# Kernel optimization log

Measured on AMD Instinct MI355X. Metric: run time of the kernel, lower is better.

The kernel has to match this reference:

```python
import math
import jax, jax.numpy as jnp
import numpy as np

H = 16          # head_count
DM = 1024       # model_dim
D = DM // H     # dim_per_head = 64
B, SL, CL = 2, 1024, 512


def setup_inputs() -> dict:
    key = jax.random.key(0)
    ks = jax.random.split(key, 16)
    s = 0.02  # weight init scale
    def W(k):
        return jax.random.normal(k, (DM, DM), jnp.float32) * s
    def b(k):
        return jax.random.normal(k, (DM,), jnp.float32) * s
    return {
        "self_kvq": jax.random.normal(ks[0], (B, SL, DM), jnp.float32),
        "ctx_kv": jax.random.normal(ks[1], (B, CL, DM), jnp.float32),
        "self_mask": jax.random.bernoulli(ks[2], 0.1, (B, SL, SL)),
        "ctx_mask": jax.random.bernoulli(ks[3], 0.1, (B, 1, CL)),
        "Wq": W(ks[4]), "bq": b(ks[5]),
        "Wks": W(ks[6]), "bks": b(ks[7]),
        "Wvs": W(ks[8]), "bvs": b(ks[9]),
        "Wkc": W(ks[10]), "bkc": b(ks[11]),
        "Wvc": W(ks[12]), "bvc": b(ks[13]),
        "ctx_bias": jnp.full((1,), -10.0, jnp.float32),  # Parameter(ones(1) * -10)
        "Wo": W(ks[14]), "bo": b(ks[15]),
    }


def reference(self_kvq, ctx_kv, self_mask, ctx_mask,
              Wq, bq, Wks, bks, Wvs, bvs, Wkc, bkc, Wvc, bvc,
              ctx_bias, Wo, bo):
    Bx, self_len, _ = self_kvq.shape
    ctx_len = ctx_kv.shape[1]

    def shape4(x):  # (B, L, DM) -> (B, H, L, D)
        return x.reshape(Bx, -1, H, D).transpose(0, 2, 1, 3)

    query = shape4(self_kvq @ Wq.T + bq) / math.sqrt(D)
    key = shape4(jnp.concatenate([self_kvq @ Wks.T + bks, ctx_kv @ Wkc.T + bkc], axis=1))
    value = shape4(jnp.concatenate([self_kvq @ Wvs.T + bvs, ctx_kv @ Wvc.T + bvc], axis=1))

    scores = jnp.einsum('bhqd,bhkd->bhqk', query, key)
    # ctx_weight_param: add learned bias to the context segment of the scores
    kidx = jnp.arange(self_len + ctx_len)
    scores = scores + jnp.where(kidx >= self_len, ctx_bias[0], jnp.zeros((), scores.dtype))
    scores = scores.astype(jnp.float32)

    # self_mask: (B, Q, self_len) -> (B, 1, Q, self_len); ctx_mask: (B, 1, ctx_len) -> (B, 1, Q, ctx_len)
    full_mask = jnp.concatenate([
        jnp.broadcast_to(self_mask[:, None], (Bx, 1, self_len, self_len)),
        jnp.broadcast_to(ctx_mask[:, None], (Bx, 1, self_len, ctx_len)),
    ], axis=-1)
    scores = jnp.where(full_mask, jnp.float32(-1e18), scores)

    attn = jax.nn.softmax(scores, axis=-1).astype(query.dtype)
    # dropout p=0.0 -> identity
    context = jnp.einsum('bhqk,bhkd->bhqd', attn, value)
    context = context.transpose(0, 2, 1, 3).reshape(Bx, self_len, H * D)
    output = context @ Wo.T + bo

    ctx_attn_probs = attn[..., self_len:]
    ctx_attn_probs = ctx_attn_probs / ctx_attn_probs.sum(axis=-1, keepdims=True)
    top_attn = ctx_attn_probs[:, 0]  # head 0: (B, Q, ctx_len)
    return output, top_attn, attn
```

## Files before the change

kernel.cpp:

```cpp
#include <hip/hip_runtime.h>
#include <cstdint>

constexpr int H  = 16;
constexpr int D  = 64;
constexpr int DM = 1024;
constexpr int B  = 2;
constexpr int SL = 1024;
constexpr int CL = 512;
constexpr int KL = SL + CL;
constexpr int SPAD = KL + 4;
constexpr size_t M1 = 1u << 20;

typedef short bf16x8  __attribute__((ext_vector_type(8)));
typedef float f32x4   __attribute__((ext_vector_type(4)));
typedef short short4v __attribute__((ext_vector_type(4)));

__device__ __forceinline__ short f2b(float f) {
    uint32_t u = __float_as_uint(f);
    u = (u + 0x7fffu + ((u >> 16) & 1u)) >> 16;
    return (short)u;
}

__device__ __forceinline__ bf16x8 ld8(const unsigned short* p) {
    return *reinterpret_cast<const bf16x8*>(p);
}

__device__ __forceinline__ void async16(const void* g, void* l) {
    __builtin_amdgcn_global_load_lds(
        (const __attribute__((address_space(1))) void*)g,
        (__attribute__((address_space(3))) void*)l,
        16, 0, 0);
}

struct ConvSrc { const float* p[8]; };

__global__ __launch_bounds__(256)
void convert_kernel(ConvSrc srcs, unsigned short* __restrict__ dst)
{
    size_t i8 = (size_t)blockIdx.x * 256 + threadIdx.x;
    size_t e  = i8 * 8;
    int u = (int)(e >> 20);
    const float* s; size_t off;
    if (u < 2) { s = srcs.p[0]; off = e; }
    else       { s = srcs.p[u - 1]; off = e - ((size_t)u << 20); }
    float4 a = *reinterpret_cast<const float4*>(s + off);
    float4 b = *reinterpret_cast<const float4*>(s + off + 4);
    bf16x8 r;
    r[0]=f2b(a.x); r[1]=f2b(a.y); r[2]=f2b(a.z); r[3]=f2b(a.w);
    r[4]=f2b(b.x); r[5]=f2b(b.y); r[6]=f2b(b.z); r[7]=f2b(b.w);
    *reinterpret_cast<bf16x8*>(dst + e) = r;
}

template<int MODE, int RPB_SHIFT, int OUTLEN, int ROWOFF>
__device__ __forceinline__ void gemm128_body(
    const unsigned short* __restrict__ A,
    const unsigned short* __restrict__ W,
    const float* __restrict__ bias,
    void* __restrict__ outp, float scale,
    unsigned short* sA, unsigned short* sB)
{
    const int t   = threadIdx.x;
    const int l   = t & 63;
    const int wid = t >> 6;
    const int wr  = wid >> 1, wc = wid & 1;
    const int lr  = l & 15,  lg = l >> 4;
    const int mbase = blockIdx.y * 128;
    const int nbase = blockIdx.x * 128;

    f32x4 acc[4][4] = {};
    for (int k0 = 0; k0 < DM; k0 += 32) {
        #pragma unroll
        for (int i = 0; i < 2; ++i) {
            int c   = t + 256 * i;
            int row = c >> 2, kc = (c & 3) * 8;
            async16(A + (size_t)(mbase + row) * DM + k0 + kc, sA + c * 8);
            async16(W + (size_t)(nbase + row) * DM + k0 + kc, sB + c * 8);
        }
        __syncthreads();
        bf16x8 af[4], bfr[4];
        #pragma unroll
        for (int i = 0; i < 4; ++i) {
            af[i]  = ld8(sA + (wr * 64 + i * 16 + lr) * 32 + lg * 8);
            bfr[i] = ld8(sB + (wc * 64 + i * 16 + lr) * 32 + lg * 8);
        }
        #pragma unroll
        for (int i = 0; i < 4; ++i)
            #pragma unroll
            for (int j = 0; j < 4; ++j)
                acc[i][j] = __builtin_amdgcn_mfma_f32_16x16x32_bf16(af[i], bfr[j], acc[i][j], 0, 0, 0);
        __syncthreads();
    }

    #pragma unroll
    for (int mi = 0; mi < 4; ++mi) {
        #pragma unroll
        for (int nj = 0; nj < 4; ++nj) {
            int n = nbase + wc * 64 + nj * 16 + lr;
            float bi = bias[n];
            if (MODE == 1) {
                int m0 = mbase + wr * 64 + mi * 16 + lg * 4;
                int bb = m0 >> RPB_SHIFT;
                int s0 = m0 & ((1 << RPB_SHIFT) - 1);
                int hh = n >> 6, dd = n & 63;
                unsigned short* o = (unsigned short*)outp +
                    ((size_t)(bb * H + hh) * D + dd) * KL + ROWOFF + s0;
                short4v pk;
                #pragma unroll
                for (int r = 0; r < 4; ++r) pk[r] = f2b((acc[mi][nj][r] + bi) * scale);
                *reinterpret_cast<short4v*>(o) = pk;
            } else {
                #pragma unroll
                for (int r = 0; r < 4; ++r) {
                    int m = mbase + wr * 64 + mi * 16 + lg * 4 + r;
                    float v = (acc[mi][nj][r] + bi) * scale;
                    if (MODE == 0) {
                        int bb = m >> RPB_SHIFT;
                        int s  = m & ((1 << RPB_SHIFT) - 1);
                        int hh = n >> 6, dd = n & 63;
                        ((unsigned short*)outp)[((size_t)(bb * H + hh) * OUTLEN + ROWOFF + s) * D + dd]
                            = (unsigned short)f2b(v);
                    } else {
                        ((float*)outp)[(size_t)m * DM + n] = v;
                    }
                }
            }
        }
    }
}

__global__ __launch_bounds__(256)
void self_proj_kernel(const unsigned short* __restrict__ Abf,
                      const unsigned short* __restrict__ Wq,
                      const unsigned short* __restrict__ Wks,
                      const unsigned short* __restrict__ Wvs,
                      const float* __restrict__ bq,
                      const float* __restrict__ bks,
                      const float* __restrict__ bvs,
                      unsigned short* __restrict__ q_ws,
                      unsigned short* __restrict__ k_ws,
                      unsigned short* __restrict__ vT_ws)
{
    __shared__ unsigned short sA[128 * 32];
    __shared__ unsigned short sB[128 * 32];
    if (blockIdx.z == 0)
        gemm128_body<0, 10, SL, 0>(Abf, Wq,  bq,  q_ws,  0.125f, sA, sB);
    else if (blockIdx.z == 1)
        gemm128_body<0, 10, KL, 0>(Abf, Wks, bks, k_ws,  1.0f,   sA, sB);
    else
        gemm128_body<1, 10, 0,  0>(Abf, Wvs, bvs, vT_ws, 1.0f,   sA, sB);
}

__global__ __launch_bounds__(256)
void ctx_proj_kernel(const unsigned short* __restrict__ Abf,
                     const unsigned short* __restrict__ Wkc,
                     const unsigned short* __restrict__ Wvc,
                     const float* __restrict__ bkc,
                     const float* __restrict__ bvc,
                     unsigned short* __restrict__ k_ws,
                     unsigned short* __restrict__ vT_ws)
{
    __shared__ unsigned short sA[128 * 32];
    __shared__ unsigned short sB[128 * 32];
    if (blockIdx.z == 0)
        gemm128_body<0, 9, KL, SL>(Abf, Wkc, bkc, k_ws,  1.0f, sA, sB);
    else
        gemm128_body<1, 9, 0,  SL>(Abf, Wvc, bvc, vT_ws, 1.0f, sA, sB);
}

__global__ __launch_bounds__(256)
void out_proj_kernel(const unsigned short* __restrict__ ctx_bf,
                     const unsigned short* __restrict__ Wo,
                     const float* __restrict__ bo,
                     float* __restrict__ out0)
{
    __shared__ unsigned short sA[128 * 32];
    __shared__ unsigned short sB[128 * 32];
    gemm128_body<2, 10, 0, 0>(ctx_bf, Wo, bo, out0, 1.0f, sA, sB);
}

__global__ __launch_bounds__(512)
void attn_kernel(const unsigned short* __restrict__ q_ws,
                 const unsigned short* __restrict__ k_ws,
                 const unsigned short* __restrict__ vT_ws,
                 const int* __restrict__ self_mask,
                 const int* __restrict__ ctx_mask,
                 const float* __restrict__ ctx_bias,
                 float* __restrict__ attn_out,
                 float* __restrict__ top_out,
                 unsigned short* __restrict__ ctx_ws)
{
    __shared__ float s_scores[16 * SPAD];
    __shared__ float s_rden[16];

    const int bid = blockIdx.x;
    const int bh  = bid & 31;
    const int qt  = bid >> 5;
    const int b   = bh >> 4;
    const int h   = bh & 15;
    const int t   = threadIdx.x;
    const int l   = t & 63;
    const int wid = t >> 6;
    const int lr  = l & 15;
    const int lg  = l >> 4;

    const unsigned short* qb = q_ws + (size_t)bh * SL * D + (size_t)qt * 16 * D;
    const unsigned short* kb = k_ws + (size_t)bh * KL * D;
    const unsigned short* vb = vT_ws + (size_t)bh * D * KL;

    bf16x8 aq0 = ld8(qb + lr * D + lg * 8);
    bf16x8 aq1 = ld8(qb + lr * D + 32 + lg * 8);

    for (int jj = 0; jj < 12; ++jj) {
        int j  = wid * 12 + jj;
        int kp = j * 16 + lr;
        bf16x8 bk0 = ld8(kb + (size_t)kp * D + lg * 8);
        bf16x8 bk1 = ld8(kb + (size_t)kp * D + 32 + lg * 8);
        f32x4 c = {};
        c = __builtin_amdgcn_mfma_f32_16x16x32_bf16(aq0, bk0, c, 0, 0, 0);
        c = __builtin_amdgcn_mfma_f32_16x16x32_bf16(aq1, bk1, c, 0, 0, 0);
        #pragma unroll
        for (int r = 0; r < 4; ++r)
            s_scores[(lg * 4 + r) * SPAD + j * 16 + lr] = c[r];
    }
    __syncthreads();

    {
        const int rr = t >> 5;
        const int c0 = t & 31;
        const int qg = qt * 16 + rr;
        const float cb = ctx_bias[0];
        const int4* smrow4 = (const int4*)(self_mask + ((size_t)b * SL + qg) * SL);
        const int4* cmrow4 = (const int4*)(ctx_mask + (size_t)b * CL);
        float* srow = s_scores + rr * SPAD;

        float4 ev[12];
        float mx = -3.0e38f;
        #pragma unroll
        for (int jj = 0; jj < 12; ++jj) {
            int c4 = c0 + jj * 32;
            float4 s = *reinterpret_cast<const float4*>(srow + c4 * 4);
            if (c4 < 256) {
                int4 m = smrow4[c4];
                if (m.x) s.x = -1e30f;
                if (m.y) s.y = -1e30f;
                if (m.z) s.z = -1e30f;
                if (m.w) s.w = -1e30f;
            } else {
                int4 m = cmrow4[c4 - 256];
                s.x += cb; s.y += cb; s.z += cb; s.w += cb;
                if (m.x) s.x = -1e30f;
                if (m.y) s.y = -1e30f;
                if (m.z) s.z = -1e30f;
                if (m.w) s.w = -1e30f;
            }
            ev[jj] = s;
            mx = fmaxf(mx, fmaxf(fmaxf(s.x, s.y), fmaxf(s.z, s.w)));
        }
        #pragma unroll
        for (int o = 1; o < 32; o <<= 1) mx = fmaxf(mx, __shfl_xor(mx, o));

        float sum = 0.f, csum = 0.f;
        #pragma unroll
        for (int jj = 0; jj < 12; ++jj) {
            int c4 = c0 + jj * 32;
            float4 s = ev[jj];
            float4 e;
            e.x = __expf(s.x - mx); e.y = __expf(s.y - mx);
            e.z = __expf(s.z - mx); e.w = __expf(s.w - mx);
            ev[jj] = e;
            *reinterpret_cast<float4*>(srow + c4 * 4) = e;
            float se = e.x + e.y + e.z + e.w;
            sum += se;
            if (c4 >= 256) csum += se;
        }
        #pragma unroll
        for (int o = 1; o < 32; o <<= 1) { sum += __shfl_xor(sum, o); csum += __shfl_xor(csum, o); }
        float rden = 1.0f / sum;
        float rcs  = 1.0f / csum;
        if (c0 == 0) s_rden[rr] = rden;

        float4* arow4 = (float4*)(attn_out + ((size_t)bh * SL + qg) * KL);
        float4* trow4 = (float4*)(top_out + ((size_t)b * SL + qg) * CL);
        #pragma unroll
        for (int jj = 0; jj < 12; ++jj) {
            int c4 = c0 + jj * 32;
            float4 e = ev[jj];
            float4 w; w.x = e.x * rden; w.y = e.y * rden; w.z = e.z * rden; w.w = e.w * rden;
            arow4[c4] = w;
            if (h == 0 && c4 >= 256) {
                float4 tw; tw.x = e.x * rcs; tw.y = e.y * rcs; tw.z = e.z * rcs; tw.w = e.w * rcs;
                trow4[c4 - 256] = tw;
            }
        }
    }
    __syncthreads();

    f32x4 accv[4] = {};
    for (int ks = 0; ks < 6; ++ks) {
        int k0 = wid * 192 + ks * 32;
        const float* prow = s_scores + lr * SPAD + k0 + lg * 8;
        float4 p0 = *reinterpret_cast<const float4*>(prow);
        float4 p1 = *reinterpret_cast<const float4*>(prow + 4);
        bf16x8 ap;
        ap[0]=f2b(p0.x); ap[1]=f2b(p0.y); ap[2]=f2b(p0.z); ap[3]=f2b(p0.w);
        ap[4]=f2b(p1.x); ap[5]=f2b(p1.y); ap[6]=f2b(p1.z); ap[7]=f2b(p1.w);
        #pragma unroll
        for (int df = 0; df < 4; ++df) {
            bf16x8 bv = ld8(vb + (size_t)(df * 16 + lr) * KL + k0 + lg * 8);
            accv[df] = __builtin_amdgcn_mfma_f32_16x16x32_bf16(ap, bv, accv[df], 0, 0, 0);
        }
    }
    __syncthreads();
    float* s_part = s_scores;
    #pragma unroll
    for (int df = 0; df < 4; ++df)
        #pragma unroll
        for (int r = 0; r < 4; ++r)
            s_part[wid * 1024 + (lg * 4 + r) * 64 + df * 16 + lr] = accv[df][r];
    __syncthreads();

    for (int i = t; i < 1024; i += 512) {
        int s = i >> 6, dd = i & 63;
        float v = 0.f;
        #pragma unroll
        for (int w = 0; w < 8; ++w) v += s_part[w * 1024 + i];
        v *= s_rden[s];
        ctx_ws[((size_t)b * SL + (size_t)qt * 16 + s) * DM + h * D + dd] = (unsigned short)f2b(v);
    }
}

extern "C" void kernel_launch(void* const* d_in, const int* in_sizes, int n_in,
                              void* d_out, int out_size, void* d_ws, size_t ws_size,
                              hipStream_t stream)
{
    const float* self_kvq = (const float*)d_in[0];
    const float* ctx_kv   = (const float*)d_in[1];
    const int*   self_mask= (const int*)d_in[2];
    const int*   ctx_mask = (const int*)d_in[3];
    const float* Wq  = (const float*)d_in[4];
    const float* bq  = (const float*)d_in[5];
    const float* Wks = (const float*)d_in[6];
    const float* bks = (const float*)d_in[7];
    const float* Wvs = (const float*)d_in[8];
    const float* bvs = (const float*)d_in[9];
    const float* Wkc = (const float*)d_in[10];
    const float* bkc = (const float*)d_in[11];
    const float* Wvc = (const float*)d_in[12];
    const float* bvc = (const float*)d_in[13];
    const float* ctx_bias = (const float*)d_in[14];
    const float* Wo  = (const float*)d_in[15];
    const float* bo  = (const float*)d_in[16];

    float* out0     = (float*)d_out;
    float* out_top  = out0 + (size_t)B * SL * DM;
    float* out_attn = out_top + (size_t)B * SL * CL;

    unsigned short* wsp  = (unsigned short*)d_ws;
    unsigned short* Abf_self = wsp + 0 * M1;
    unsigned short* Abf_ctx  = wsp + 2 * M1;
    unsigned short* Wq_b     = wsp + 3 * M1;
    unsigned short* Wks_b    = wsp + 4 * M1;
    unsigned short* Wvs_b    = wsp + 5 * M1;
    unsigned short* Wkc_b    = wsp + 6 * M1;
    unsigned short* Wvc_b    = wsp + 7 * M1;
    unsigned short* Wo_b     = wsp + 8 * M1;
    unsigned short* q_ws     = wsp + 9 * M1;
    unsigned short* k_ws     = wsp + 11 * M1;
    unsigned short* vT_ws    = wsp + 14 * M1;
    unsigned short* ctx_ws   = wsp + 0;

    ConvSrc cs;
    cs.p[0] = self_kvq; cs.p[1] = ctx_kv;
    cs.p[2] = Wq; cs.p[3] = Wks; cs.p[4] = Wvs;
    cs.p[5] = Wkc; cs.p[6] = Wvc; cs.p[7] = Wo;
    convert_kernel<<<4608, 256, 0, stream>>>(cs, wsp);

    self_proj_kernel<<<dim3(8, 16, 3), 256, 0, stream>>>(
        Abf_self, Wq_b, Wks_b, Wvs_b, bq, bks, bvs, q_ws, k_ws, vT_ws);
    ctx_proj_kernel<<<dim3(8, 8, 2), 256, 0, stream>>>(
        Abf_ctx, Wkc_b, Wvc_b, bkc, bvc, k_ws, vT_ws);

    attn_kernel<<<dim3(2048), 512, 0, stream>>>(q_ws, k_ws, vT_ws,
        self_mask, ctx_mask, ctx_bias, out_attn, out_top, ctx_ws);

    out_proj_kernel<<<dim3(8, 16), 256, 0, stream>>>(ctx_ws, Wo_b, bo, out0);
}
```

Measured before the change: 445.7 us.

## Rework attention softmax into two-pass recompute, merge projections, retile GEMMs with swizzle

The attention kernel now packs masks into LDS bitmasks, computes an online max/sum in a first QK pass, then recomputes scores in a second pass to write normalized probabilities directly. It stores bf16 probabilities in LDS instead of fp32 scores and reduces PV partials with LDS atomics. The GEMMs move to 64x128 tiles with K=64 steps and XOR-swizzled shared memory, and the self and context projections merge into one launch. This is meant to cut LDS footprint for occupancy, drop a kernel launch, and reduce bank conflicts, at the price of doing QK twice.

```diff
diff --git a/kernel.cpp b/kernel.cpp
--- a/kernel.cpp
+++ b/kernel.cpp
@@ -8,7 +8,7 @@
 constexpr int SL = 1024;
 constexpr int CL = 512;
 constexpr int KL = SL + CL;
-constexpr int SPAD = KL + 4;
+constexpr int EPAD = 1540;
 constexpr size_t M1 = 1u << 20;
 
 typedef short bf16x8  __attribute__((ext_vector_type(8)));
@@ -52,53 +52,67 @@
 }
 
 template<int MODE, int RPB_SHIFT, int OUTLEN, int ROWOFF>
-__device__ __forceinline__ void gemm128_body(
+__device__ __forceinline__ void gemm_body(
     const unsigned short* __restrict__ A,
     const unsigned short* __restrict__ W,
     const float* __restrict__ bias,
     void* __restrict__ outp, float scale,
-    unsigned short* sA, unsigned short* sB)
+    unsigned short* sA, unsigned short* sB, int by, int bx)
 {
     const int t   = threadIdx.x;
     const int l   = t & 63;
     const int wid = t >> 6;
-    const int wr  = wid >> 1, wc = wid & 1;
-    const int lr  = l & 15,  lg = l >> 4;
-    const int mbase = blockIdx.y * 128;
-    const int nbase = blockIdx.x * 128;
-
-    f32x4 acc[4][4] = {};
-    for (int k0 = 0; k0 < DM; k0 += 32) {
+    const int lr  = l & 15, lg = l >> 4;
+    const int mbase = by * 64;
+    const int nbase = bx * 128;
+
+    f32x4 acc[4][2] = {};
+    for (int k0 = 0; k0 < DM; k0 += 64) {
         #pragma unroll
         for (int i = 0; i < 2; ++i) {
-            int c   = t + 256 * i;
-            int row = c >> 2, kc = (c & 3) * 8;
-            async16(A + (size_t)(mbase + row) * DM + k0 + kc, sA + c * 8);
-            async16(W + (size_t)(nbase + row) * DM + k0 + kc, sB + c * 8);
+            int c = t + 256 * i;
+            int row = c >> 3, gd = (c & 7) ^ (row & 7);
+            async16(A + (size_t)(mbase + row) * DM + k0 + gd * 8, sA + c * 8);
+        }
+        #pragma unroll
+        for (int i = 0; i < 4; ++i) {
+            int c = t + 256 * i;
+            int row = c >> 3, gd = (c & 7) ^ (row & 7);
+            async16(W + (size_t)(nbase + row) * DM + k0 + gd * 8, sB + c * 8);
         }
         __syncthreads();
-        bf16x8 af[4], bfr[4];
-        #pragma unroll
-        for (int i = 0; i < 4; ++i) {
-            af[i]  = ld8(sA + (wr * 64 + i * 16 + lr) * 32 + lg * 8);
-            bfr[i] = ld8(sB + (wc * 64 + i * 16 + lr) * 32 + lg * 8);
-        }
-        #pragma unroll
-        for (int i = 0; i < 4; ++i)
+        bf16x8 af[4][2], bfr[2][2];
+        #pragma unroll
+        for (int s = 0; s < 2; ++s) {
             #pragma unroll
-            for (int j = 0; j < 4; ++j)
-                acc[i][j] = __builtin_amdgcn_mfma_f32_16x16x32_bf16(af[i], bfr[j], acc[i][j], 0, 0, 0);
+            for (int i = 0; i < 4; ++i) {
+                int row = i * 16 + lr;
+                af[i][s] = ld8(sA + (row * 8 + ((s * 4 + lg) ^ (row & 7))) * 8);
+            }
+            #pragma unroll
+            for (int j = 0; j < 2; ++j) {
+                int row = wid * 32 + j * 16 + lr;
+                bfr[j][s] = ld8(sB + (row * 8 + ((s * 4 + lg) ^ (row & 7))) * 8);
+            }
+        }
+        #pragma unroll
+        for (int s = 0; s < 2; ++s)
+            #pragma unroll
+            for (int i = 0; i < 4; ++i)
+                #pragma unroll
+                for (int j = 0; j < 2; ++j)
+                    acc[i][j] = __builtin_amdgcn_mfma_f32_16x16x32_bf16(af[i][s], bfr[j][s], acc[i][j], 0, 0, 0);
         __syncthreads();
     }
 
     #pragma unroll
     for (int mi = 0; mi < 4; ++mi) {
         #pragma unroll
-        for (int nj = 0; nj < 4; ++nj) {
-            int n = nbase + wc * 64 + nj * 16 + lr;
+        for (int nj = 0; nj < 2; ++nj) {
+            int n = nbase + wid * 32 + nj * 16 + lr;
             float bi = bias[n];
             if (MODE == 1) {
-                int m0 = mbase + wr * 64 + mi * 16 + lg * 4;
+                int m0 = mbase + mi * 16 + lg * 4;
                 int bb = m0 >> RPB_SHIFT;
                 int s0 = m0 & ((1 << RPB_SHIFT) - 1);
                 int hh = n >> 6, dd = n & 63;
@@ -111,7 +125,7 @@
             } else {
                 #pragma unroll
                 for (int r = 0; r < 4; ++r) {
-                    int m = mbase + wr * 64 + mi * 16 + lg * 4 + r;
+                    int m = mbase + mi * 16 + lg * 4 + r;
                     float v = (acc[mi][nj][r] + bi) * scale;
                     if (MODE == 0) {
                         int bb = m >> RPB_SHIFT;
@@ -120,7 +134,7 @@
                         ((unsigned short*)outp)[((size_t)(bb * H + hh) * OUTLEN + ROWOFF + s) * D + dd]
                             = (unsigned short)f2b(v);
                     } else {
-                        ((float*)outp)[(size_t)m * DM + n] = v;
+                        __builtin_nontemporal_store(v, (float*)outp + (size_t)m * DM + n);
                     }
                 }
             }
@@ -129,42 +143,36 @@
 }
 
 __global__ __launch_bounds__(256)
-void self_proj_kernel(const unsigned short* __restrict__ Abf,
-                      const unsigned short* __restrict__ Wq,
-                      const unsigned short* __restrict__ Wks,
-                      const unsigned short* __restrict__ Wvs,
-                      const float* __restrict__ bq,
-                      const float* __restrict__ bks,
-                      const float* __restrict__ bvs,
-                      unsigned short* __restrict__ q_ws,
-                      unsigned short* __restrict__ k_ws,
-                      unsigned short* __restrict__ vT_ws)
-{
-    __shared__ unsigned short sA[128 * 32];
-    __shared__ unsigned short sB[128 * 32];
-    if (blockIdx.z == 0)
-        gemm128_body<0, 10, SL, 0>(Abf, Wq,  bq,  q_ws,  0.125f, sA, sB);
-    else if (blockIdx.z == 1)
-        gemm128_body<0, 10, KL, 0>(Abf, Wks, bks, k_ws,  1.0f,   sA, sB);
+void proj_kernel(const unsigned short* __restrict__ Aself,
+                 const unsigned short* __restrict__ Actx,
+                 const unsigned short* __restrict__ Wq,
+                 const unsigned short* __restrict__ Wks,
+                 const unsigned short* __restrict__ Wvs,
+                 const unsigned short* __restrict__ Wkc,
+                 const unsigned short* __restrict__ Wvc,
+                 const float* __restrict__ bq,  const float* __restrict__ bks,
+                 const float* __restrict__ bvs, const float* __restrict__ bkc,
+                 const float* __restrict__ bvc,
+                 unsigned short* __restrict__ q_ws,
+                 unsigned short* __restrict__ k_ws,
+                 unsigned short* __restrict__ vT_ws)
+{
+    __shared__ unsigned short sA[64 * 64];
+    __shared__ unsigned short sB[128 * 64];
+    int bid = blockIdx.x;
+    int z, by, bx;
+    if (bid < 768) { z = bid >> 8; int r = bid & 255; by = r >> 3; bx = r & 7; }
+    else { int tt = bid - 768; z = 3 + (tt >> 7); int r = tt & 127; by = r >> 3; bx = r & 7; }
+    if (z == 0)
+        gemm_body<0, 10, SL, 0 >(Aself, Wq,  bq,  q_ws,  0.125f, sA, sB, by, bx);
+    else if (z == 1)
+        gemm_body<0, 10, KL, 0 >(Aself, Wks, bks, k_ws,  1.0f,   sA, sB, by, bx);
+    else if (z == 2)
+        gemm_body<1, 10, 0,  0 >(Aself, Wvs, bvs, vT_ws, 1.0f,   sA, sB, by, bx);
+    else if (z == 3)
+        gemm_body<0, 9,  KL, SL>(Actx,  Wkc, bkc, k_ws,  1.0f,   sA, sB, by, bx);
     else
-        gemm128_body<1, 10, 0,  0>(Abf, Wvs, bvs, vT_ws, 1.0f,   sA, sB);
-}
-
-__global__ __launch_bounds__(256)
-void ctx_proj_kernel(const unsigned short* __restrict__ Abf,
-                     const unsigned short* __restrict__ Wkc,
-                     const unsigned short* __restrict__ Wvc,
-                     const float* __restrict__ bkc,
-                     const float* __restrict__ bvc,
-                     unsigned short* __restrict__ k_ws,
-                     unsigned short* __restrict__ vT_ws)
-{
-    __shared__ unsigned short sA[128 * 32];
-    __shared__ unsigned short sB[128 * 32];
-    if (blockIdx.z == 0)
-        gemm128_body<0, 9, KL, SL>(Abf, Wkc, bkc, k_ws,  1.0f, sA, sB);
-    else
-        gemm128_body<1, 9, 0,  SL>(Abf, Wvc, bvc, vT_ws, 1.0f, sA, sB);
+        gemm_body<1, 9,  0,  SL>(Actx,  Wvc, bvc, vT_ws, 1.0f,   sA, sB, by, bx);
 }
 
 __global__ __launch_bounds__(256)
@@ -173,12 +181,12 @@
                      const float* __restrict__ bo,
                      float* __restrict__ out0)
 {
-    __shared__ unsigned short sA[128 * 32];
-    __shared__ unsigned short sB[128 * 32];
-    gemm128_body<2, 10, 0, 0>(ctx_bf, Wo, bo, out0, 1.0f, sA, sB);
-}
-
-__global__ __launch_bounds__(512)
+    __shared__ unsigned short sA[64 * 64];
+    __shared__ unsigned short sB[128 * 64];
+    gemm_body<2, 10, 0, 0>(ctx_bf, Wo, bo, out0, 1.0f, sA, sB, blockIdx.y, blockIdx.x);
+}
+
+__global__ __launch_bounds__(512, 4)
 void attn_kernel(const unsigned short* __restrict__ q_ws,
                  const unsigned short* __restrict__ k_ws,
                  const unsigned short* __restrict__ vT_ws,
@@ -189,8 +197,11 @@
                  float* __restrict__ top_out,
                  unsigned short* __restrict__ ctx_ws)
 {
-    __shared__ float s_scores[16 * SPAD];
-    __shared__ float s_rden[16];
+    __shared__ unsigned short e_lds[16 * EPAD];
+    __shared__ float s_part[16 * 64];
+    __shared__ unsigned int mb[16 * 48];
+    __shared__ float wred[16 * 8 * 3];
+    __shared__ float fin[16 * 3];
 
     const int bid = blockIdx.x;
     const int bh  = bid & 31;
@@ -202,130 +213,167 @@
     const int wid = t >> 6;
     const int lr  = l & 15;
     const int lg  = l >> 4;
-
-    const unsigned short* qb = q_ws + (size_t)bh * SL * D + (size_t)qt * 16 * D;
+    const int qrow0 = qt * 16;
+
+    {
+        int row = t >> 5, w = t & 31;
+        const int4* p = (const int4*)(self_mask + ((size_t)b * SL + qrow0 + row) * SL + w * 32);
+        unsigned bits = 0;
+        #pragma unroll
+        for (int g = 0; g < 8; ++g) {
+            int4 v = p[g];
+            bits |= (unsigned)(v.x != 0) << (g * 4);
+            bits |= (unsigned)(v.y != 0) << (g * 4 + 1);
+            bits |= (unsigned)(v.z != 0) << (g * 4 + 2);
+            bits |= (unsigned)(v.w != 0) << (g * 4 + 3);
+        }
+        mb[row * 48 + w] = bits;
+    }
+    if (t < 256) {
+        int row = t >> 4, w = t & 15;
+        const int4* p = (const int4*)(ctx_mask + (size_t)b * CL + w * 32);
+        unsigned bits = 0;
+        #pragma unroll
+        for (int g = 0; g < 8; ++g) {
+            int4 v = p[g];
+            bits |= (unsigned)(v.x != 0) << (g * 4);
+            bits |= (unsigned)(v.y != 0) << (g * 4 + 1);
+            bits |= (unsigned)(v.z != 0) << (g * 4 + 2);
+            bits |= (unsigned)(v.w != 0) << (g * 4 + 3);
+        }
+        mb[row * 48 + 32 + w] = bits;
+    }
+    s_part[t] = 0.f;
+    s_part[t + 512] = 0.f;
+
+    const unsigned short* qb = q_ws + ((size_t)bh * SL + qrow0) * D;
     const unsigned short* kb = k_ws + (size_t)bh * KL * D;
-    const unsigned short* vb = vT_ws + (size_t)bh * D * KL;
-
+    const float cb = ctx_bias[0];
     bf16x8 aq0 = ld8(qb + lr * D + lg * 8);
     bf16x8 aq1 = ld8(qb + lr * D + 32 + lg * 8);
+    __syncthreads();
+
+    float m[4], sa[4], sc[4];
+    #pragma unroll
+    for (int r = 0; r < 4; ++r) { m[r] = -3.0e38f; sa[r] = 0.f; sc[r] = 0.f; }
 
     for (int jj = 0; jj < 12; ++jj) {
-        int j  = wid * 12 + jj;
-        int kp = j * 16 + lr;
-        bf16x8 bk0 = ld8(kb + (size_t)kp * D + lg * 8);
-        bf16x8 bk1 = ld8(kb + (size_t)kp * D + 32 + lg * 8);
+        int j = wid * 12 + jj;
+        int col = j * 16 + lr;
+        bf16x8 bk0 = ld8(kb + (size_t)col * D + lg * 8);
+        bf16x8 bk1 = ld8(kb + (size_t)col * D + 32 + lg * 8);
         f32x4 c = {};
         c = __builtin_amdgcn_mfma_f32_16x16x32_bf16(aq0, bk0, c, 0, 0, 0);
         c = __builtin_amdgcn_mfma_f32_16x16x32_bf16(aq1, bk1, c, 0, 0, 0);
-        #pragma unroll
-        for (int r = 0; r < 4; ++r)
-            s_scores[(lg * 4 + r) * SPAD + j * 16 + lr] = c[r];
+        const int isctx = (col >= SL);
+        const int wi = col >> 5, bit = col & 31;
+        #pragma unroll
+        for (int r = 0; r < 4; ++r) {
+            int row = lg * 4 + r;
+            float v = c[r] + (isctx ? cb : 0.f);
+            if ((mb[row * 48 + wi] >> bit) & 1u) v = -1e30f;
+            float nm = fmaxf(m[r], v);
+            float rs = __expf(m[r] - nm);
+            float ev = __expf(v - nm);
+            sa[r] = sa[r] * rs + ev;
+            sc[r] = sc[r] * rs + (isctx ? ev : 0.f);
+            m[r]  = nm;
+        }
+    }
+    #pragma unroll
+    for (int off = 1; off < 16; off <<= 1) {
+        #pragma unroll
+        for (int r = 0; r < 4; ++r) {
+            float om = __shfl_xor(m[r], off);
+            float os = __shfl_xor(sa[r], off);
+            float oc = __shfl_xor(sc[r], off);
+            float nm = fmaxf(m[r], om);
+            float e1 = __expf(m[r] - nm), e2 = __expf(om - nm);
+            sa[r] = sa[r] * e1 + os * e2;
+            sc[r] = sc[r] * e1 + oc * e2;
+            m[r]  = nm;
+        }
+    }
+    if (lr == 0) {
+        #pragma unroll
+        for (int r = 0; r < 4; ++r) {
+            int row = lg * 4 + r;
+            wred[(row * 8 + wid) * 3 + 0] = m[r];
+            wred[(row * 8 + wid) * 3 + 1] = sa[r];
+            wred[(row * 8 + wid) * 3 + 2] = sc[r];
+        }
     }
     __syncthreads();
-
-    {
-        const int rr = t >> 5;
-        const int c0 = t & 31;
-        const int qg = qt * 16 + rr;
-        const float cb = ctx_bias[0];
-        const int4* smrow4 = (const int4*)(self_mask + ((size_t)b * SL + qg) * SL);
-        const int4* cmrow4 = (const int4*)(ctx_mask + (size_t)b * CL);
-        float* srow = s_scores + rr * SPAD;
-
-        float4 ev[12];
-        float mx = -3.0e38f;
-        #pragma unroll
-        for (int jj = 0; jj < 12; ++jj) {
-            int c4 = c0 + jj * 32;
-            float4 s = *reinterpret_cast<const float4*>(srow + c4 * 4);
-            if (c4 < 256) {
-                int4 m = smrow4[c4];
-                if (m.x) s.x = -1e30f;
-                if (m.y) s.y = -1e30f;
-                if (m.z) s.z = -1e30f;
-                if (m.w) s.w = -1e30f;
-            } else {
-                int4 m = cmrow4[c4 - 256];
-                s.x += cb; s.y += cb; s.z += cb; s.w += cb;
-                if (m.x) s.x = -1e30f;
-                if (m.y) s.y = -1e30f;
-                if (m.z) s.z = -1e30f;
-                if (m.w) s.w = -1e30f;
+    if (t < 16) {
+        float fm = -3.0e38f, fs = 0.f, fc = 0.f;
+        #pragma unroll
+        for (int w = 0; w < 8; ++w) {
+            float wm = wred[(t * 8 + w) * 3 + 0];
+            float ws = wred[(t * 8 + w) * 3 + 1];
+            float wc = wred[(t * 8 + w) * 3 + 2];
+            float nm = fmaxf(fm, wm);
+            float e1 = __expf(fm - nm), e2 = __expf(wm - nm);
+            fs = fs * e1 + ws * e2;
+            fc = fc * e1 + wc * e2;
+            fm = nm;
+        }
+        fin[t * 3 + 0] = fm;
+        fin[t * 3 + 1] = 1.0f / fs;
+        fin[t * 3 + 2] = 1.0f / fc;
+    }
+    __syncthreads();
+
+    float* aout = attn_out + ((size_t)bh * SL + qrow0) * KL;
+    float* tout = top_out + ((size_t)b * SL + qrow0) * CL;
+    for (int jj = 0; jj < 12; ++jj) {
+        int j = wid * 12 + jj;
+        int col = j * 16 + lr;
+        bf16x8 bk0 = ld8(kb + (size_t)col * D + lg * 8);
+        bf16x8 bk1 = ld8(kb + (size_t)col * D + 32 + lg * 8);
+        f32x4 c = {};
+        c = __builtin_amdgcn_mfma_f32_16x16x32_bf16(aq0, bk0, c, 0, 0, 0);
+        c = __builtin_amdgcn_mfma_f32_16x16x32_bf16(aq1, bk1, c, 0, 0, 0);
+        const int isctx = (col >= SL);
+        const int wi = col >> 5, bit = col & 31;
+        #pragma unroll
+        for (int r = 0; r < 4; ++r) {
+            int row = lg * 4 + r;
+            float v = c[r] + (isctx ? cb : 0.f);
+            if ((mb[row * 48 + wi] >> bit) & 1u) v = -1e30f;
+            float ev = __expf(v - fin[row * 3 + 0]);
+            float p  = ev * fin[row * 3 + 1];
+            __builtin_nontemporal_store(p, aout + (size_t)row * KL + col);
+            e_lds[row * EPAD + col] = (unsigned short)f2b(p);
+            if (h == 0 && isctx) {
+                float tp = ev * fin[row * 3 + 2];
+                __builtin_nontemporal_store(tp, tout + (size_t)row * CL + (col - SL));
             }
-            ev[jj] = s;
-            mx = fmaxf(mx, fmaxf(fmaxf(s.x, s.y), fmaxf(s.z, s.w)));
-        }
-        #pragma unroll
-        for (int o = 1; o < 32; o <<= 1) mx = fmaxf(mx, __shfl_xor(mx, o));
-
-        float sum = 0.f, csum = 0.f;
-        #pragma unroll
-        for (int jj = 0; jj < 12; ++jj) {
-            int c4 = c0 + jj * 32;
-            float4 s = ev[jj];
-            float4 e;
-            e.x = __expf(s.x - mx); e.y = __expf(s.y - mx);
-            e.z = __expf(s.z - mx); e.w = __expf(s.w - mx);
-            ev[jj] = e;
-            *reinterpret_cast<float4*>(srow + c4 * 4) = e;
-            float se = e.x + e.y + e.z + e.w;
-            sum += se;
-            if (c4 >= 256) csum += se;
-        }
-        #pragma unroll
-        for (int o = 1; o < 32; o <<= 1) { sum += __shfl_xor(sum, o); csum += __shfl_xor(csum, o); }
-        float rden = 1.0f / sum;
-        float rcs  = 1.0f / csum;
-        if (c0 == 0) s_rden[rr] = rden;
-
-        float4* arow4 = (float4*)(attn_out + ((size_t)bh * SL + qg) * KL);
-        float4* trow4 = (float4*)(top_out + ((size_t)b * SL + qg) * CL);
-        #pragma unroll
-        for (int jj = 0; jj < 12; ++jj) {
-            int c4 = c0 + jj * 32;
-            float4 e = ev[jj];
-            float4 w; w.x = e.x * rden; w.y = e.y * rden; w.z = e.z * rden; w.w = e.w * rden;
-            arow4[c4] = w;
-            if (h == 0 && c4 >= 256) {
-                float4 tw; tw.x = e.x * rcs; tw.y = e.y * rcs; tw.z = e.z * rcs; tw.w = e.w * rcs;
-                trow4[c4 - 256] = tw;
-            }
         }
     }
     __syncthreads();
 
+    const unsigned short* vb = vT_ws + (size_t)bh * D * KL;
     f32x4 accv[4] = {};
     for (int ks = 0; ks < 6; ++ks) {
         int k0 = wid * 192 + ks * 32;
-        const float* prow = s_scores + lr * SPAD + k0 + lg * 8;
-        float4 p0 = *reinterpret_cast<const float4*>(prow);
-        float4 p1 = *reinterpret_cast<const float4*>(prow + 4);
-        bf16x8 ap;
-        ap[0]=f2b(p0.x); ap[1]=f2b(p0.y); ap[2]=f2b(p0.z); ap[3]=f2b(p0.w);
-        ap[4]=f2b(p1.x); ap[5]=f2b(p1.y); ap[6]=f2b(p1.z); ap[7]=f2b(p1.w);
+        bf16x8 ap = ld8(e_lds + lr * EPAD + k0 + lg * 8);
         #pragma unroll
         for (int df = 0; df < 4; ++df) {
             bf16x8 bv = ld8(vb + (size_t)(df * 16 + lr) * KL + k0 + lg * 8);
             accv[df] = __builtin_amdgcn_mfma_f32_16x16x32_bf16(ap, bv, accv[df], 0, 0, 0);
         }
     }
-    __syncthreads();
-    float* s_part = s_scores;
     #pragma unroll
     for (int df = 0; df < 4; ++df)
         #pragma unroll
         for (int r = 0; r < 4; ++r)
-            s_part[wid * 1024 + (lg * 4 + r) * 64 + df * 16 + lr] = accv[df][r];
+            atomicAdd(&s_part[(lg * 4 + r) * 64 + df * 16 + lr], accv[df][r]);
     __syncthreads();
 
     for (int i = t; i < 1024; i += 512) {
-        int s = i >> 6, dd = i & 63;
-        float v = 0.f;
-        #pragma unroll
-        for (int w = 0; w < 8; ++w) v += s_part[w * 1024 + i];
-        v *= s_rden[s];
-        ctx_ws[((size_t)b * SL + (size_t)qt * 16 + s) * DM + h * D + dd] = (unsigned short)f2b(v);
+        int srow = i >> 6, dd = i & 63;
+        ctx_ws[((size_t)b * SL + qrow0 + srow) * DM + h * D + dd]
+            = (unsigned short)f2b(s_part[i]);
     }
 }
 
@@ -375,13 +423,12 @@
     cs.p[5] = Wkc; cs.p[6] = Wvc; cs.p[7] = Wo;
     convert_kernel<<<4608, 256, 0, stream>>>(cs, wsp);
 
-    self_proj_kernel<<<dim3(8, 16, 3), 256, 0, stream>>>(
-        Abf_self, Wq_b, Wks_b, Wvs_b, bq, bks, bvs, q_ws, k_ws, vT_ws);
-    ctx_proj_kernel<<<dim3(8, 8, 2), 256, 0, stream>>>(
-        Abf_ctx, Wkc_b, Wvc_b, bkc, bvc, k_ws, vT_ws);
+    proj_kernel<<<dim3(1024), 256, 0, stream>>>(
+        Abf_self, Abf_ctx, Wq_b, Wks_b, Wvs_b, Wkc_b, Wvc_b,
+        bq, bks, bvs, bkc, bvc, q_ws, k_ws, vT_ws);
 
     attn_kernel<<<dim3(2048), 512, 0, stream>>>(q_ws, k_ws, vT_ws,
         self_mask, ctx_mask, ctx_bias, out_attn, out_top, ctx_ws);
 
-    out_proj_kernel<<<dim3(8, 16), 256, 0, stream>>>(ctx_ws, Wo_b, bo, out0);
-}
+    out_proj_kernel<<<dim3(8, 32), 256, 0, stream>>>(ctx_ws, Wo_b, bo, out0);
+}
```

Result: slower. 526.9 us (+18.2%).

## Merge projection launches, widen GEMM K-step with swizzled LDS, restructure attention for 1024 threads

Applied to the files above, without the earlier changes.

The self and context projection GEMMs become one launch, and the GEMM now loads 64-wide K slices into an XOR-swizzled LDS layout to avoid bank conflicts. The output projection uses 64-row tiles to put more blocks in flight. The attention kernel moves to 1024 threads with one wave per query row. It writes normalized bf16 probabilities to LDS for the PV MFMA, reduces partial results with LDS atomics, and uses nontemporal stores for the large attn and output writes. The aim is to cut launch overhead, LDS conflicts and cache pollution, at the cost of more LDS per block and atomic contention.

```diff
diff --git a/kernel.cpp b/kernel.cpp
--- a/kernel.cpp
+++ b/kernel.cpp
@@ -8,7 +8,8 @@
 constexpr int SL = 1024;
 constexpr int CL = 512;
 constexpr int KL = SL + CL;
-constexpr int SPAD = KL + 4;
+constexpr int SPAD = 1540;
+constexpr int EPAD = 1544;
 constexpr size_t M1 = 1u << 20;
 
 typedef short bf16x8  __attribute__((ext_vector_type(8)));
@@ -30,6 +31,10 @@
         (const __attribute__((address_space(1))) void*)g,
         (__attribute__((address_space(3))) void*)l,
         16, 0, 0);
+}
+
+__device__ __forceinline__ void nt_store4(f32x4 v, float* p) {
+    __builtin_nontemporal_store(v, (f32x4*)p);
 }
 
 struct ConvSrc { const float* p[8]; };
@@ -51,54 +56,68 @@
     *reinterpret_cast<bf16x8*>(dst + e) = r;
 }
 
-template<int MODE, int RPB_SHIFT, int OUTLEN, int ROWOFF>
-__device__ __forceinline__ void gemm128_body(
+template<int BM, int MODE, int RPB_SHIFT, int OUTLEN, int ROWOFF>
+__device__ __forceinline__ void gemm_body(
     const unsigned short* __restrict__ A,
     const unsigned short* __restrict__ W,
     const float* __restrict__ bias,
     void* __restrict__ outp, float scale,
-    unsigned short* sA, unsigned short* sB)
-{
+    unsigned short* sA, unsigned short* sB, int by, int bx)
+{
+    constexpr int MFRAG = BM / 32;
     const int t   = threadIdx.x;
     const int l   = t & 63;
     const int wid = t >> 6;
     const int wr  = wid >> 1, wc = wid & 1;
-    const int lr  = l & 15,  lg = l >> 4;
-    const int mbase = blockIdx.y * 128;
-    const int nbase = blockIdx.x * 128;
-
-    f32x4 acc[4][4] = {};
-    for (int k0 = 0; k0 < DM; k0 += 32) {
-        #pragma unroll
-        for (int i = 0; i < 2; ++i) {
-            int c   = t + 256 * i;
-            int row = c >> 2, kc = (c & 3) * 8;
-            async16(A + (size_t)(mbase + row) * DM + k0 + kc, sA + c * 8);
-            async16(W + (size_t)(nbase + row) * DM + k0 + kc, sB + c * 8);
+    const int lr  = l & 15, lg = l >> 4;
+    const int mbase = by * BM;
+    const int nbase = bx * 128;
+
+    f32x4 acc[MFRAG][4] = {};
+    for (int k0 = 0; k0 < DM; k0 += 64) {
+        #pragma unroll
+        for (int i = 0; i < MFRAG; ++i) {
+            int c = t + 256 * i;
+            int row = c >> 3, gd = (c & 7) ^ (row & 7);
+            async16(A + (size_t)(mbase + row) * DM + k0 + gd * 8, sA + c * 8);
+        }
+        #pragma unroll
+        for (int i = 0; i < 4; ++i) {
+            int c = t + 256 * i;
+            int row = c >> 3, gd = (c & 7) ^ (row & 7);
+            async16(W + (size_t)(nbase + row) * DM + k0 + gd * 8, sB + c * 8);
         }
         __syncthreads();
-        bf16x8 af[4], bfr[4];
-        #pragma unroll
-        for (int i = 0; i < 4; ++i) {
-            af[i]  = ld8(sA + (wr * 64 + i * 16 + lr) * 32 + lg * 8);
-            bfr[i] = ld8(sB + (wc * 64 + i * 16 + lr) * 32 + lg * 8);
-        }
-        #pragma unroll
-        for (int i = 0; i < 4; ++i)
+        #pragma unroll
+        for (int s = 0; s < 2; ++s) {
+            bf16x8 af[MFRAG], bfr[4];
             #pragma unroll
-            for (int j = 0; j < 4; ++j)
-                acc[i][j] = __builtin_amdgcn_mfma_f32_16x16x32_bf16(af[i], bfr[j], acc[i][j], 0, 0, 0);
+            for (int i = 0; i < MFRAG; ++i) {
+                int row = wr * (BM / 2) + i * 16 + lr;
+                af[i] = ld8(sA + (row * 8 + ((s * 4 + lg) ^ (row & 7))) * 8);
+            }
+            #pragma unroll
+            for (int j = 0; j < 4; ++j) {
+                int row = wc * 64 + j * 16 + lr;
+                bfr[j] = ld8(sB + (row * 8 + ((s * 4 + lg) ^ (row & 7))) * 8);
+            }
+            #pragma unroll
+            for (int i = 0; i < MFRAG; ++i)
+                #pragma unroll
+                for (int j = 0; j < 4; ++j)
+                    acc[i][j] = __builtin_amdgcn_mfma_f32_16x16x32_bf16(af[i], bfr[j], acc[i][j], 0, 0, 0);
+        }
         __syncthreads();
     }
 
     #pragma unroll
-    for (int mi = 0; mi < 4; ++mi) {
+    for (int mi = 0; mi < MFRAG; ++mi) {
         #pragma unroll
         for (int nj = 0; nj < 4; ++nj) {
             int n = nbase + wc * 64 + nj * 16 + lr;
             float bi = bias[n];
             if (MODE == 1) {
-                int m0 = mbase + wr * 64 + mi * 16 + lg * 4;
+                int m0 = mbase + wr * (BM / 2) + mi * 16 + lg * 4;
                 int bb = m0 >> RPB_SHIFT;
                 int s0 = m0 & ((1 << RPB_SHIFT) - 1);
                 int hh = n >> 6, dd = n & 63;
@@ -111,7 +130,7 @@
             } else {
                 #pragma unroll
                 for (int r = 0; r < 4; ++r) {
-                    int m = mbase + wr * 64 + mi * 16 + lg * 4 + r;
+                    int m = mbase + wr * (BM / 2) + mi * 16 + lg * 4 + r;
                     float v = (acc[mi][nj][r] + bi) * scale;
                     if (MODE == 0) {
                         int bb = m >> RPB_SHIFT;
@@ -120,7 +139,7 @@
                         ((unsigned short*)outp)[((size_t)(bb * H + hh) * OUTLEN + ROWOFF + s) * D + dd]
                             = (unsigned short)f2b(v);
                     } else {
-                        ((float*)outp)[(size_t)m * DM + n] = v;
+                        __builtin_nontemporal_store(v, (float*)outp + (size_t)m * DM + n);
                     }
                 }
             }
@@ -128,57 +147,51 @@
     }
 }
 
-__global__ __launch_bounds__(256)
-void self_proj_kernel(const unsigned short* __restrict__ Abf,
-                      const unsigned short* __restrict__ Wq,
-                      const unsigned short* __restrict__ Wks,
-                      const unsigned short* __restrict__ Wvs,
-                      const float* __restrict__ bq,
-                      const float* __restrict__ bks,
-                      const float* __restrict__ bvs,
-                      unsigned short* __restrict__ q_ws,
-                      unsigned short* __restrict__ k_ws,
-                      unsigned short* __restrict__ vT_ws)
-{
-    __shared__ unsigned short sA[128 * 32];
-    __shared__ unsigned short sB[128 * 32];
-    if (blockIdx.z == 0)
-        gemm128_body<0, 10, SL, 0>(Abf, Wq,  bq,  q_ws,  0.125f, sA, sB);
-    else if (blockIdx.z == 1)
-        gemm128_body<0, 10, KL, 0>(Abf, Wks, bks, k_ws,  1.0f,   sA, sB);
+__global__ __launch_bounds__(256, 2)
+void proj_kernel(const unsigned short* __restrict__ Aself,
+                 const unsigned short* __restrict__ Actx,
+                 const unsigned short* __restrict__ Wq,
+                 const unsigned short* __restrict__ Wks,
+                 const unsigned short* __restrict__ Wvs,
+                 const unsigned short* __restrict__ Wkc,
+                 const unsigned short* __restrict__ Wvc,
+                 const float* __restrict__ bq,  const float* __restrict__ bks,
+                 const float* __restrict__ bvs, const float* __restrict__ bkc,
+                 const float* __restrict__ bvc,
+                 unsigned short* __restrict__ q_ws,
+                 unsigned short* __restrict__ k_ws,
+                 unsigned short* __restrict__ vT_ws)
+{
+    __shared__ unsigned short sA[128 * 64];
+    __shared__ unsigned short sB[128 * 64];
+    int bid = blockIdx.x;
+    int z, by, bx;
+    if (bid < 384) { z = bid >> 7; int r = bid & 127; by = r >> 3; bx = r & 7; }
+    else { int tt = bid - 384; z = 3 + (tt >> 6); int r = tt & 63; by = r >> 3; bx = r & 7; }
+    if (z == 0)
+        gemm_body<128, 0, 10, SL, 0 >(Aself, Wq,  bq,  q_ws,  0.125f, sA, sB, by, bx);
+    else if (z == 1)
+        gemm_body<128, 0, 10, KL, 0 >(Aself, Wks, bks, k_ws,  1.0f,   sA, sB, by, bx);
+    else if (z == 2)
+        gemm_body<128, 1, 10, 0,  0 >(Aself, Wvs, bvs, vT_ws, 1.0f,   sA, sB, by, bx);
+    else if (z == 3)
+        gemm_body<128, 0, 9,  KL, SL>(Actx,  Wkc, bkc, k_ws,  1.0f,   sA, sB, by, bx);
     else
-        gemm128_body<1, 10, 0,  0>(Abf, Wvs, bvs, vT_ws, 1.0f,   sA, sB);
-}
-
-__global__ __launch_bounds__(256)
-void ctx_proj_kernel(const unsigned short* __restrict__ Abf,
-                     const unsigned short* __restrict__ Wkc,
-                     const unsigned short* __restrict__ Wvc,
-                     const float* __restrict__ bkc,
-                     const float* __restrict__ bvc,
-                     unsigned short* __restrict__ k_ws,
-                     unsigned short* __restrict__ vT_ws)
-{
-    __shared__ unsigned short sA[128 * 32];
-    __shared__ unsigned short sB[128 * 32];
-    if (blockIdx.z == 0)
-        gemm128_body<0, 9, KL, SL>(Abf, Wkc, bkc, k_ws,  1.0f, sA, sB);
-    else
-        gemm128_body<1, 9, 0,  SL>(Abf, Wvc, bvc, vT_ws, 1.0f, sA, sB);
-}
-
-__global__ __launch_bounds__(256)
+        gemm_body<128, 1, 9,  0,  SL>(Actx,  Wvc, bvc, vT_ws, 1.0f,   sA, sB, by, bx);
+}
+
+__global__ __launch_bounds__(256, 2)
 void out_proj_kernel(const unsigned short* __restrict__ ctx_bf,
                      const unsigned short* __restrict__ Wo,
                      const float* __restrict__ bo,
                      float* __restrict__ out0)
 {
-    __shared__ unsigned short sA[128 * 32];
-    __shared__ unsigned short sB[128 * 32];
-    gemm128_body<2, 10, 0, 0>(ctx_bf, Wo, bo, out0, 1.0f, sA, sB);
-}
-
-__global__ __launch_bounds__(512)
+    __shared__ unsigned short sA[64 * 64];
+    __shared__ unsigned short sB[128 * 64];
+    gemm_body<64, 2, 10, 0, 0>(ctx_bf, Wo, bo, out0, 1.0f, sA, sB, blockIdx.y, blockIdx.x);
+}
+
+__global__ __launch_bounds__(1024, 4)
 void attn_kernel(const unsigned short* __restrict__ q_ws,
                  const unsigned short* __restrict__ k_ws,
                  const unsigned short* __restrict__ vT_ws,
@@ -190,7 +203,8 @@
                  unsigned short* __restrict__ ctx_ws)
 {
     __shared__ float s_scores[16 * SPAD];
-    __shared__ float s_rden[16];
+    __shared__ unsigned short e_lds[16 * EPAD];
+    __shared__ float s_part[16 * 65];
 
     const int bid = blockIdx.x;
     const int bh  = bid & 31;
@@ -202,51 +216,53 @@
     const int wid = t >> 6;
     const int lr  = l & 15;
     const int lg  = l >> 4;
-
-    const unsigned short* qb = q_ws + (size_t)bh * SL * D + (size_t)qt * 16 * D;
+    const int qrow0 = qt * 16;
+
+    s_part[t] = 0.f;
+    if (t < 16) s_part[1024 + t] = 0.f;
+
+    const unsigned short* qb = q_ws + ((size_t)bh * SL + qrow0) * D;
     const unsigned short* kb = k_ws + (size_t)bh * KL * D;
-    const unsigned short* vb = vT_ws + (size_t)bh * D * KL;
-
     bf16x8 aq0 = ld8(qb + lr * D + lg * 8);
     bf16x8 aq1 = ld8(qb + lr * D + 32 + lg * 8);
 
-    for (int jj = 0; jj < 12; ++jj) {
-        int j  = wid * 12 + jj;
-        int kp = j * 16 + lr;
-        bf16x8 bk0 = ld8(kb + (size_t)kp * D + lg * 8);
-        bf16x8 bk1 = ld8(kb + (size_t)kp * D + 32 + lg * 8);
+    #pragma unroll
+    for (int jj = 0; jj < 6; ++jj) {
+        int j = wid * 6 + jj;
+        int col = j * 16 + lr;
+        bf16x8 bk0 = ld8(kb + (size_t)col * D + lg * 8);
+        bf16x8 bk1 = ld8(kb + (size_t)col * D + 32 + lg * 8);
         f32x4 c = {};
         c = __builtin_amdgcn_mfma_f32_16x16x32_bf16(aq0, bk0, c, 0, 0, 0);
         c = __builtin_amdgcn_mfma_f32_16x16x32_bf16(aq1, bk1, c, 0, 0, 0);
         #pragma unroll
         for (int r = 0; r < 4; ++r)
-            s_scores[(lg * 4 + r) * SPAD + j * 16 + lr] = c[r];
+            s_scores[(lg * 4 + r) * SPAD + col] = c[r];
     }
     __syncthreads();
 
     {
-        const int rr = t >> 5;
-        const int c0 = t & 31;
-        const int qg = qt * 16 + rr;
+        const int row = wid;
+        const int qg  = qrow0 + row;
         const float cb = ctx_bias[0];
-        const int4* smrow4 = (const int4*)(self_mask + ((size_t)b * SL + qg) * SL);
-        const int4* cmrow4 = (const int4*)(ctx_mask + (size_t)b * CL);
-        float* srow = s_scores + rr * SPAD;
-
-        float4 ev[12];
+        const int4* sm4 = (const int4*)(self_mask + ((size_t)b * SL + qg) * SL);
+        const int4* cm4 = (const int4*)(ctx_mask + (size_t)b * CL);
+        float* srow = s_scores + row * SPAD;
+
+        float4 ev[6];
         float mx = -3.0e38f;
         #pragma unroll
-        for (int jj = 0; jj < 12; ++jj) {
-            int c4 = c0 + jj * 32;
+        for (int jj = 0; jj < 6; ++jj) {
+            int c4 = l + jj * 64;
             float4 s = *reinterpret_cast<const float4*>(srow + c4 * 4);
-            if (c4 < 256) {
-                int4 m = smrow4[c4];
+            if (jj < 4) {
+                int4 m = sm4[c4];
                 if (m.x) s.x = -1e30f;
                 if (m.y) s.y = -1e30f;
                 if (m.z) s.z = -1e30f;
                 if (m.w) s.w = -1e30f;
             } else {
-                int4 m = cmrow4[c4 - 256];
+                int4 m = cm4[c4 - 256];
                 s.x += cb; s.y += cb; s.z += cb; s.w += cb;
                 if (m.x) s.x = -1e30f;
                 if (m.y) s.y = -1e30f;
@@ -257,75 +273,72 @@
             mx = fmaxf(mx, fmaxf(fmaxf(s.x, s.y), fmaxf(s.z, s.w)));
         }
         #pragma unroll
-        for (int o = 1; o < 32; o <<= 1) mx = fmaxf(mx, __shfl_xor(mx, o));
+        for (int o = 1; o < 64; o <<= 1) mx = fmaxf(mx, __shfl_xor(mx, o));
 
         float sum = 0.f, csum = 0.f;
         #pragma unroll
-        for (int jj = 0; jj < 12; ++jj) {
-            int c4 = c0 + jj * 32;
+        for (int jj = 0; jj < 6; ++jj) {
             float4 s = ev[jj];
             float4 e;
             e.x = __expf(s.x - mx); e.y = __expf(s.y - mx);
             e.z = __expf(s.z - mx); e.w = __expf(s.w - mx);
             ev[jj] = e;
-            *reinterpret_cast<float4*>(srow + c4 * 4) = e;
             float se = e.x + e.y + e.z + e.w;
             sum += se;
-            if (c4 >= 256) csum += se;
-        }
-        #pragma unroll
-        for (int o = 1; o < 32; o <<= 1) { sum += __shfl_xor(sum, o); csum += __shfl_xor(csum, o); }
+            if (jj >= 4) csum += se;
+        }
+        #pragma unroll
+        for (int o = 1; o < 64; o <<= 1) { sum += __shfl_xor(sum, o); csum += __shfl_xor(csum, o); }
         float rden = 1.0f / sum;
         float rcs  = 1.0f / csum;
-        if (c0 == 0) s_rden[rr] = rden;
-
-        float4* arow4 = (float4*)(attn_out + ((size_t)bh * SL + qg) * KL);
-        float4* trow4 = (float4*)(top_out + ((size_t)b * SL + qg) * CL);
-        #pragma unroll
-        for (int jj = 0; jj < 12; ++jj) {
-            int c4 = c0 + jj * 32;
+
+        float* arow = attn_out + ((size_t)bh * SL + qg) * KL;
+        #pragma unroll
+        for (int jj = 0; jj < 6; ++jj) {
+            int c4 = l + jj * 64;
             float4 e = ev[jj];
-            float4 w; w.x = e.x * rden; w.y = e.y * rden; w.z = e.z * rden; w.w = e.w * rden;
-            arow4[c4] = w;
-            if (h == 0 && c4 >= 256) {
-                float4 tw; tw.x = e.x * rcs; tw.y = e.y * rcs; tw.z = e.z * rcs; tw.w = e.w * rcs;
-                trow4[c4 - 256] = tw;
+            f32x4 w; w[0] = e.x * rden; w[1] = e.y * rden; w[2] = e.z * rden; w[3] = e.w * rden;
+            nt_store4(w, arow + c4 * 4);
+            short4v pk;
+            pk[0] = f2b(w[0]); pk[1] = f2b(w[1]); pk[2] = f2b(w[2]); pk[3] = f2b(w[3]);
+            *reinterpret_cast<short4v*>(e_lds + (size_t)row * EPAD + c4 * 4) = pk;
+        }
+        if (h == 0) {
+            float* trow = top_out + ((size_t)b * SL + qg) * CL;
+            #pragma unroll
+            for (int jj = 4; jj < 6; ++jj) {
+                int c4 = l + jj * 64;
+                float4 e = ev[jj];
+                f32x4 w; w[0] = e.x * rcs; w[1] = e.y * rcs; w[2] = e.z * rcs; w[3] = e.w * rcs;
+                nt_store4(w, trow + (c4 - 256) * 4);
             }
         }
     }
     __syncthreads();
 
+    const unsigned short* vb = vT_ws + (size_t)bh * D * KL;
     f32x4 accv[4] = {};
-    for (int ks = 0; ks < 6; ++ks) {
-        int k0 = wid * 192 + ks * 32;
-        const float* prow = s_scores + lr * SPAD + k0 + lg * 8;
-        float4 p0 = *reinterpret_cast<const float4*>(prow);
-        float4 p1 = *reinterpret_cast<const float4*>(prow + 4);
-        bf16x8 ap;
-        ap[0]=f2b(p0.x); ap[1]=f2b(p0.y); ap[2]=f2b(p0.z); ap[3]=f2b(p0.w);
-        ap[4]=f2b(p1.x); ap[5]=f2b(p1.y); ap[6]=f2b(p1.z); ap[7]=f2b(p1.w);
+    #pragma unroll
+    for (int ks = 0; ks < 3; ++ks) {
+        int k0 = wid * 96 + ks * 32;
+        bf16x8 ap = ld8(e_lds + (size_t)lr * EPAD + k0 + lg * 8);
         #pragma unroll
         for (int df = 0; df < 4; ++df) {
             bf16x8 bv = ld8(vb + (size_t)(df * 16 + lr) * KL + k0 + lg * 8);
             accv[df] = __builtin_amdgcn_mfma_f32_16x16x32_bf16(ap, bv, accv[df], 0, 0, 0);
         }
     }
-    __syncthreads();
-    float* s_part = s_scores;
     #pragma unroll
     for (int df = 0; df < 4; ++df)
         #pragma unroll
         for (int r = 0; r < 4; ++r)
-            s_part[wid * 1024 + (lg * 4 + r) * 64 + df * 16 + lr] = accv[df][r];
+            atomicAdd(&s_part[(lg * 4 + r) * 65 + df * 16 + lr], accv[df][r]);
     __syncthreads();
 
-    for (int i = t; i < 1024; i += 512) {
-        int s = i >> 6, dd = i & 63;
-        float v = 0.f;
-        #pragma unroll
-        for (int w = 0; w < 8; ++w) v += s_part[w * 1024 + i];
-        v *= s_rden[s];
-        ctx_ws[((size_t)b * SL + (size_t)qt * 16 + s) * DM + h * D + dd] = (unsigned short)f2b(v);
+    {
+        int srow = t >> 6, dd = t & 63;
+        ctx_ws[((size_t)b * SL + qrow0 + srow) * DM + h * D + dd]
+            = (unsigned short)f2b(s_part[srow * 65 + dd]);
     }
 }
 
@@ -375,13 +388,12 @@
     cs.p[5] = Wkc; cs.p[6] = Wvc; cs.p[7] = Wo;
     convert_kernel<<<4608, 256, 0, stream>>>(cs, wsp);
 
-    self_proj_kernel<<<dim3(8, 16, 3), 256, 0, stream>>>(
-        Abf_self, Wq_b, Wks_b, Wvs_b, bq, bks, bvs, q_ws, k_ws, vT_ws);
-    ctx_proj_kernel<<<dim3(8, 8, 2), 256, 0, stream>>>(
-        Abf_ctx, Wkc_b, Wvc_b, bkc, bvc, k_ws, vT_ws);
-
-    attn_kernel<<<dim3(2048), 512, 0, stream>>>(q_ws, k_ws, vT_ws,
+    proj_kernel<<<dim3(512), 256, 0, stream>>>(
+        Abf_self, Abf_ctx, Wq_b, Wks_b, Wvs_b, Wkc_b, Wvc_b,
+        bq, bks, bvs, bkc, bvc, q_ws, k_ws, vT_ws);
+
+    attn_kernel<<<dim3(2048), 1024, 0, stream>>>(q_ws, k_ws, vT_ws,
         self_mask, ctx_mask, ctx_bias, out_attn, out_top, ctx_ws);
 
-    out_proj_kernel<<<dim3(8, 16), 256, 0, stream>>>(ctx_ws, Wo_b, bo, out0);
-}
+    out_proj_kernel<<<dim3(8, 32), 256, 0, stream>>>(ctx_ws, Wo_b, bo, out0);
+}
```

Result: slower. 547.2 us (+22.8%).
